# Kernel tuning notes

Hardware: AMD Instinct MI355X
Metric: run time of the kernel (lower is better)

## Reference

```python
import jax, jax.numpy as jnp
import numpy as np

N_NODES = 100000
N_EDGES = 1600000
IN_C, HID_C, OUT_C = 128, 256, 47


def setup_inputs() -> dict:
    key = jax.random.key(0)
    ks = jax.random.split(key, 8)
    x = jax.random.normal(ks[0], (N_NODES, IN_C), dtype=jnp.float32)
    edge_index = jax.random.randint(ks[1], (2, N_EDGES), 0, N_NODES, dtype=jnp.int64)

    def glorot(k, fan_in, fan_out):
        s = 1.0 / np.sqrt(fan_in)
        return jax.random.uniform(k, (fan_in, fan_out), jnp.float32, -s, s)

    W1_l = glorot(ks[2], IN_C, HID_C)
    b1 = jnp.zeros((HID_C,), jnp.float32)
    W1_r = glorot(ks[3], IN_C, HID_C)
    W2_l = glorot(ks[4], HID_C, OUT_C)
    b2 = jnp.zeros((OUT_C,), jnp.float32)
    W2_r = glorot(ks[5], HID_C, OUT_C)
    return {"x": x, "edge_index": edge_index,
            "W1_l": W1_l, "b1": b1, "W1_r": W1_r,
            "W2_l": W2_l, "b2": b2, "W2_r": W2_r}


def _sage_conv(x, src, dst, W_l, b, W_r, num_nodes):
    # mean aggregation of source-node features onto destination nodes
    msg_sum = jax.ops.segment_sum(x[src], dst, num_segments=num_nodes)  # [N, C]
    cnt = jax.ops.segment_sum(jnp.ones((src.shape[0], 1), x.dtype), dst,
                              num_segments=num_nodes)                   # [N, 1]
    mean = msg_sum / jnp.maximum(cnt, 1.0)
    # out = lin_l(mean) + lin_r(x_root); lin_l carries the bias (PyG default)
    return mean @ W_l + b + x @ W_r


def reference(x, edge_index, W1_l, b1, W1_r, W2_l, b2, W2_r):
    num_nodes = x.shape[0]
    src, dst = edge_index[0], edge_index[1]
    h = _sage_conv(x, src, dst, W1_l, b1, W1_r, num_nodes)
    h = jax.nn.relu(h)  # dropout is identity in eval mode
    out = _sage_conv(h, src, dst, W2_l, b2, W2_r, num_nodes)
    return jax.nn.log_softmax(out, axis=-1)
```

## Files before the change

kernel.cpp:

```cpp
#include <hip/hip_runtime.h>
#include <hip/hip_bf16.h>

constexpr int IN_C  = 128;
constexpr int HID_C = 256;
constexpr int OUT_C = 47;

typedef __attribute__((ext_vector_type(8))) short bf16x8;
typedef __attribute__((ext_vector_type(4))) float f32x4;

static __device__ __forceinline__ unsigned short f2bf(float v) {
  __hip_bfloat16 hb = __float2bfloat16(v);
  return *(unsigned short*)&hb;
}
static __device__ __forceinline__ float bf2f(unsigned short u) {
  return __uint_as_float((unsigned)u << 16);
}


__global__ __launch_bounds__(256) void count_edges(const int* __restrict__ dst,
                                                   int* __restrict__ cnt, int E) {
  int e = blockIdx.x * blockDim.x + threadIdx.x;
  const int stride = gridDim.x * blockDim.x;
  for (; e < E; e += stride) {
    const int d = __builtin_nontemporal_load(&dst[e]);
    atomicAdd(&cnt[d], 1);
  }
}

__global__ __launch_bounds__(256) void scan_partials(const int* __restrict__ cnt,
                                                     int* __restrict__ part, int N) {
  const int i0 = blockIdx.x * 1024 + threadIdx.x * 4;
  int s = 0;
  if (i0 + 3 < N) {
    const int4 v = *(const int4*)&cnt[i0];
    s = v.x + v.y + v.z + v.w;
  } else {
    for (int k = 0; k < 4; ++k) { const int i = i0 + k; if (i < N) s += cnt[i]; }
  }
  #pragma unroll
  for (int o = 32; o > 0; o >>= 1) s += __shfl_xor(s, o, 64);
  __shared__ int ws[4];
  if ((threadIdx.x & 63) == 0) ws[threadIdx.x >> 6] = s;
  __syncthreads();
  if (threadIdx.x == 0) part[blockIdx.x] = ws[0] + ws[1] + ws[2] + ws[3];
}

__global__ __launch_bounds__(1024) void scan_roots(int* __restrict__ part,
                                                   int* __restrict__ off, int nb, int N) {
  __shared__ int tmp[1024];
  const int t = threadIdx.x;
  const int v = (t < nb) ? part[t] : 0;
  tmp[t] = v;
  __syncthreads();
  for (int d = 1; d < 1024; d <<= 1) {
    const int u = (t >= d) ? tmp[t - d] : 0;
    __syncthreads();
    tmp[t] += u;
    __syncthreads();
  }
  if (t < nb) part[t] = tmp[t] - v;
  if (t == 1023) off[N] = tmp[1023];
}

__global__ __launch_bounds__(256) void scan_write(const int* __restrict__ cnt,
                                                  const int* __restrict__ part,
                                                  int* __restrict__ off, int N) {
  const int b = blockIdx.x;
  const int i0 = b * 1024 + threadIdx.x * 4;
  int4 v = make_int4(0, 0, 0, 0);
  if (i0 + 3 < N) v = *(const int4*)&cnt[i0];
  else {
    int* p = (int*)&v;
    for (int k = 0; k < 4; ++k) { const int i = i0 + k; if (i < N) p[k] = cnt[i]; }
  }
  const int tsum = v.x + v.y + v.z + v.w;
  const int lane = threadIdx.x & 63;
  int incl = tsum;
  #pragma unroll
  for (int o = 1; o < 64; o <<= 1) {
    const int u = __shfl_up(incl, o, 64);
    if (lane >= o) incl += u;
  }
  __shared__ int wsum[4];
  const int wv = threadIdx.x >> 6;
  if (lane == 63) wsum[wv] = incl;
  __syncthreads();
  int wbase = 0;
  for (int w = 0; w < wv; ++w) wbase += wsum[w];
  const int tbase = part[b] + wbase + incl - tsum;
  int4 ov;
  ov.x = tbase;
  ov.y = tbase + v.x;
  ov.z = tbase + v.x + v.y;
  ov.w = tbase + v.x + v.y + v.z;
  if (i0 + 3 < N) *(int4*)&off[i0] = ov;
  else {
    int* p = (int*)&ov;
    for (int k = 0; k < 4; ++k) { const int i = i0 + k; if (i < N) off[i] = p[k]; }
  }
}

__global__ __launch_bounds__(256) void fill_csr_range(const int* __restrict__ src,
                                                      const int* __restrict__ dst,
                                                      const int* __restrict__ off,
                                                      int* __restrict__ cursor,
                                                      int* __restrict__ csr,
                                                      int E, int lo, int hi) {
  int e = blockIdx.x * blockDim.x + threadIdx.x;
  const int stride = gridDim.x * blockDim.x;
  for (; e < E; e += stride) {
    const int d = __builtin_nontemporal_load(&dst[e]);
    if (d >= lo && d < hi) {
      const int s = __builtin_nontemporal_load(&src[e]);
      const int p = atomicAdd(&cursor[d], 1);
      csr[off[d] + p] = s;
    }
  }
}

__global__ void f32_to_bf16(const float* __restrict__ in, unsigned short* __restrict__ out, int n4) {
  int i = blockIdx.x * blockDim.x + threadIdx.x;
  if (i < n4) {
    float4 v = *(const float4*)&in[i * 4];
    ushort4 o;
    o.x = f2bf(v.x); o.y = f2bf(v.y); o.z = f2bf(v.z); o.w = f2bf(v.w);
    *(ushort4*)&out[i * 4] = o;
  }
}

__global__ __launch_bounds__(256) void agg1(const unsigned short* __restrict__ xb,
                                            const int* __restrict__ off,
                                            const int* __restrict__ csr,
                                            unsigned short* __restrict__ meanb, int N) {
  const int wid  = (blockIdx.x * blockDim.x + threadIdx.x) >> 6;
  const int lane = threadIdx.x & 63;
  if (wid >= N) return;
  const unsigned* xw = (const unsigned*)xb;
  const int s0 = off[wid], s1 = off[wid + 1];
  float a0 = 0.f, a1 = 0.f, b0 = 0.f, b1 = 0.f;
  float c0 = 0.f, c1 = 0.f, d0 = 0.f, d1 = 0.f;
  for (int base = s0; base < s1; base += 64) {
    const int cnt = min(64, s1 - base);
    const int idx = (lane < cnt) ? csr[base + lane] : 0;
    int e = 0;
    for (; e + 4 <= cnt; e += 4) {
      const int sA = __shfl(idx, e, 64),     sB = __shfl(idx, e + 1, 64);
      const int sC = __shfl(idx, e + 2, 64), sD = __shfl(idx, e + 3, 64);
      const unsigned uA = xw[(size_t)sA * 64 + lane];
      const unsigned uB = xw[(size_t)sB * 64 + lane];
      const unsigned uC = xw[(size_t)sC * 64 + lane];
      const unsigned uD = xw[(size_t)sD * 64 + lane];
      a0 += __uint_as_float(uA << 16); a1 += __uint_as_float(uA & 0xffff0000u);
      b0 += __uint_as_float(uB << 16); b1 += __uint_as_float(uB & 0xffff0000u);
      c0 += __uint_as_float(uC << 16); c1 += __uint_as_float(uC & 0xffff0000u);
      d0 += __uint_as_float(uD << 16); d1 += __uint_as_float(uD & 0xffff0000u);
    }
    for (; e < cnt; ++e) {
      const int sA = __shfl(idx, e, 64);
      const unsigned uA = xw[(size_t)sA * 64 + lane];
      a0 += __uint_as_float(uA << 16); a1 += __uint_as_float(uA & 0xffff0000u);
    }
  }
  const float r0 = (a0 + b0) + (c0 + d0);
  const float r1 = (a1 + b1) + (c1 + d1);
  const int deg = s1 - s0;
  const float inv = (deg > 0) ? 1.0f / (float)deg : 0.0f;
  const unsigned lo = f2bf(r0 * inv), hi = f2bf(r1 * inv);
  ((unsigned*)meanb)[(size_t)wid * 64 + lane] = lo | (hi << 16);
}

__global__ void build_w1cat_t(const float* __restrict__ Wl, const float* __restrict__ Wr,
                              unsigned short* __restrict__ BT) {
  int idx = blockIdx.x * blockDim.x + threadIdx.x;
  if (idx < 256 * 256) {
    int j = idx >> 8, k = idx & 255;
    float v = (k < 128) ? Wl[k * 256 + j] : Wr[(k - 128) * 256 + j];
    BT[idx] = f2bf(v);
  }
}
__global__ void build_w2cat_t(const float* __restrict__ Wl, const float* __restrict__ Wr,
                              unsigned short* __restrict__ BT) {
  int idx = blockIdx.x * blockDim.x + threadIdx.x;
  if (idx < 128 * 256) {
    int j = idx >> 8, k = idx & 255;
    float v = 0.f;
    if (j < OUT_C)           v = Wl[k * OUT_C + j];
    else if (j < 2 * OUT_C)  v = Wr[k * OUT_C + (j - OUT_C)];
    BT[idx] = f2bf(v);
  }
}

template<int MODE>
__global__ __launch_bounds__(256) void gemm_mfma(const unsigned short* __restrict__ A0,
                                                 const unsigned short* __restrict__ A1,
                                                 const unsigned short* __restrict__ BT,
                                                 const float* __restrict__ bias,
                                                 unsigned short* __restrict__ Out,
                                                 int M) {
  constexpr int ONC = (MODE == 0) ? 256 : 128;
  __shared__ unsigned short Asl[128 * 64];
  __shared__ unsigned short Bsl[128 * 64];
  const int tid  = threadIdx.x;
  const int wid  = tid >> 6, lane = tid & 63;
  const int wm   = wid >> 1, wn = wid & 1;
  const int r0   = blockIdx.x * 128;
  const int c0   = blockIdx.y * 128;

  f32x4 acc[4][4];
  #pragma unroll
  for (int m = 0; m < 4; ++m)
    #pragma unroll
    for (int n = 0; n < 4; ++n)
      #pragma unroll
      for (int j = 0; j < 4; ++j) acc[m][n][j] = 0.f;

  const int srow = lane >> 3;
  const int cs   = (lane & 7) ^ srow;
  const int fr   = lane & 15;
  const int klo  = (lane >> 4) * 16;
  const int swz  = (fr & 7) << 4;

  #pragma unroll 1
  for (int kb = 0; kb < 4; ++kb) {
    const unsigned short* Ap;
    int acol, ak;
    if (MODE == 0) { Ap = (kb < 2) ? A0 : A1; acol = (kb & 1) * 64; ak = 128; }
    else           { Ap = A0;                 acol = kb * 64;       ak = 256; }
    #pragma unroll
    for (int i = 0; i < 4; ++i) {
      const int rl = wid * 32 + i * 8 + srow;
      int gr = r0 + rl; if (gr > M - 1) gr = M - 1;
      const unsigned short* gsa = Ap + (size_t)gr * ak + acol + cs * 8;
      __builtin_amdgcn_global_load_lds(
          (const __attribute__((address_space(1))) unsigned int*)gsa,
          (__attribute__((address_space(3))) unsigned int*)&Asl[(wid * 32 + i * 8) * 64],
          16, 0, 0);
      const unsigned short* gsb = BT + (size_t)(c0 + rl) * 256 + kb * 64 + cs * 8;
      __builtin_amdgcn_global_load_lds(
          (const __attribute__((address_space(1))) unsigned int*)gsb,
          (__attribute__((address_space(3))) unsigned int*)&Bsl[(wid * 32 + i * 8) * 64],
          16, 0, 0);
    }
    asm volatile("s_waitcnt vmcnt(0)");
    __syncthreads();
    #pragma unroll
    for (int ks = 0; ks < 2; ++ks) {
      bf16x8 af[4], bfv[4];
      #pragma unroll
      for (int m = 0; m < 4; ++m) {
        const int ro = (wm * 64 + m * 16 + fr) * 128 + ((ks * 64 + klo) ^ swz);
        af[m] = *(const bf16x8*)((const char*)Asl + ro);
      }
      #pragma unroll
      for (int n = 0; n < 4; ++n) {
        const int ro = (wn * 64 + n * 16 + fr) * 128 + ((ks * 64 + klo) ^ swz);
        bfv[n] = *(const bf16x8*)((const char*)Bsl + ro);
      }
      #pragma unroll
      for (int m = 0; m < 4; ++m)
        #pragma unroll
        for (int n = 0; n < 4; ++n)
          acc[m][n] = __builtin_amdgcn_mfma_f32_16x16x32_bf16(af[m], bfv[n], acc[m][n], 0, 0, 0);
    }
    __syncthreads();
  }

  const int orow0 = r0 + wm * 64 + (lane >> 4) * 4;
  const int ocol0 = c0 + wn * 64 + (lane & 15);
  #pragma unroll
  for (int m = 0; m < 4; ++m) {
    #pragma unroll
    for (int n = 0; n < 4; ++n) {
      const int col = ocol0 + n * 16;
      const float badd = (MODE == 0) ? bias[col] : 0.f;
      #pragma unroll
      for (int j = 0; j < 4; ++j) {
        const int row = orow0 + m * 16 + j;
        if (row < M) {
          float v = acc[m][n][j] + badd;
          if (MODE == 0) v = fmaxf(v, 0.f);
          Out[(size_t)row * ONC + col] = f2bf(v);
        }
      }
    }
  }
}

__global__ __launch_bounds__(256) void final_kernel(const unsigned short* __restrict__ Ob,
                                                    const int* __restrict__ off,
                                                    const int* __restrict__ csr,
                                                    const float* __restrict__ b2,
                                                    float* __restrict__ out, int N) {
  const int wid  = (blockIdx.x * blockDim.x + threadIdx.x) >> 6;
  const int lane = threadIdx.x & 63;
  if (wid >= N) return;
  const int s0 = off[wid], s1 = off[wid + 1];
  const bool act = lane < OUT_C;
  const int cl = act ? lane : 0;
  float t0 = 0.f, t1 = 0.f, t2 = 0.f, t3 = 0.f;
  for (int base = s0; base < s1; base += 64) {
    const int cnt = min(64, s1 - base);
    const int idx = (lane < cnt) ? csr[base + lane] : 0;
    int e = 0;
    for (; e + 4 <= cnt; e += 4) {
      const int sA = __shfl(idx, e, 64),     sB = __shfl(idx, e + 1, 64);
      const int sC = __shfl(idx, e + 2, 64), sD = __shfl(idx, e + 3, 64);
      if (act) {
        t0 += bf2f(Ob[(size_t)sA * 128 + lane]);
        t1 += bf2f(Ob[(size_t)sB * 128 + lane]);
        t2 += bf2f(Ob[(size_t)sC * 128 + lane]);
        t3 += bf2f(Ob[(size_t)sD * 128 + lane]);
      }
    }
    for (; e < cnt; ++e) {
      const int sA = __shfl(idx, e, 64);
      if (act) t0 += bf2f(Ob[(size_t)sA * 128 + lane]);
    }
  }
  const float sum = (t0 + t1) + (t2 + t3);
  const int deg = s1 - s0;
  const float inv = (deg > 0) ? 1.0f / (float)deg : 0.0f;
  float v = sum * inv + b2[cl] + bf2f(Ob[(size_t)wid * 128 + OUT_C + cl]);
  if (!act) v = -INFINITY;
  float m = v;
  #pragma unroll
  for (int o = 32; o > 0; o >>= 1) m = fmaxf(m, __shfl_xor(m, o, 64));
  float ex = act ? expf(v - m) : 0.f;
  float s = ex;
  #pragma unroll
  for (int o = 32; o > 0; o >>= 1) s += __shfl_xor(s, o, 64);
  if (act) out[(size_t)wid * OUT_C + lane] = v - m - logf(s);
}


extern "C" void kernel_launch(void* const* d_in, const int* in_sizes, int n_in,
                              void* d_out, int out_size, void* d_ws, size_t ws_size,
                              hipStream_t stream) {
  const float* x   = (const float*)d_in[0];
  const int*   ei  = (const int*)d_in[1];
  const float* W1l = (const float*)d_in[2];
  const float* b1  = (const float*)d_in[3];
  const float* W1r = (const float*)d_in[4];
  const float* W2l = (const float*)d_in[5];
  const float* b2  = (const float*)d_in[6];
  const float* W2r = (const float*)d_in[7];
  float* out = (float*)d_out;

  const int N = in_sizes[0] / IN_C;
  const int E = in_sizes[1] / 2;
  const int* src = ei;
  const int* dst = ei + E;

  char* base = (char*)d_ws;
  size_t o = 0;
  auto take = [&](size_t bytes) -> char* {
    char* p = base + o;
    o = (o + bytes + 255) & ~(size_t)255;
    return p;
  };
  int* cnt    = (int*)take((size_t)N * 4);
  int* cursor = (int*)take((size_t)N * 4);
  const size_t zero_bytes = o;
  int* off    = (int*)take((size_t)(N + 1) * 4);
  int* part   = (int*)take((size_t)1024 * 4);
  int* csr    = (int*)take((size_t)E * 4);
  unsigned short* xb    = (unsigned short*)take((size_t)N * IN_C * 2);
  unsigned short* meanb = (unsigned short*)take((size_t)N * IN_C * 2);
  unsigned short* h     = (unsigned short*)take((size_t)N * HID_C * 2);
  unsigned short* W1T   = (unsigned short*)take((size_t)256 * 256 * 2);
  unsigned short* W2T   = (unsigned short*)take((size_t)128 * 256 * 2);
  unsigned short* Ocat  = meanb;
  (void)ws_size; (void)n_in; (void)out_size;

  hipMemsetAsync(base, 0, zero_bytes, stream);

  const int tb = 256;
  const int nb = (N + 1023) / 1024;
  count_edges<<<2048, tb, 0, stream>>>(dst, cnt, E);
  scan_partials<<<nb, 256, 0, stream>>>(cnt, part, N);
  scan_roots<<<1, 1024, 0, stream>>>(part, off, nb, N);
  scan_write<<<nb, 256, 0, stream>>>(cnt, part, off, N);

  const int P = 4;
  const int chunk = (N + P - 1) / P;
  for (int p = 0; p < P; ++p) {
    const int lo = p * chunk;
    const int hi = min(N, lo + chunk);
    fill_csr_range<<<2048, tb, 0, stream>>>(src, dst, off, cursor, csr, E, lo, hi);
  }

  const int n4 = N * IN_C / 4;
  f32_to_bf16<<<(n4 + tb - 1) / tb, tb, 0, stream>>>(x, xb, n4);
  build_w1cat_t<<<256, 256, 0, stream>>>(W1l, W1r, W1T);
  build_w2cat_t<<<128, 256, 0, stream>>>(W2l, W2r, W2T);

  agg1<<<(N + 3) / 4, 256, 0, stream>>>(xb, off, csr, meanb, N);

  const int mb = (N + 127) / 128;
  gemm_mfma<0><<<dim3(mb, 2), 256, 0, stream>>>(meanb, xb, W1T, b1, h, N);
  gemm_mfma<1><<<dim3(mb, 1), 256, 0, stream>>>(h, nullptr, W2T, nullptr, Ocat, N);

  final_kernel<<<(N + 3) / 4, 256, 0, stream>>>(Ocat, off, csr, b2, out, N);
}
```

Baseline: 475.9 us.

## Build CSR with LDS-privatized per-range histograms and block-local scatter cursors

Replaces the global-atomic edge count and the four-pass global-atomic CSR fill with a two-level scheme. Node ranges of 16384 are handled in shared memory, with 32 edge slices per range, so each block builds a private LDS histogram. A column-sum kernel turns these into per-block base offsets. The scatter kernel then uses LDS atomics on cursors seeded from the global offsets, which removes the memset and the global atomic contention. The cost is that every block rescans its whole edge slice for each of the 7 ranges, and a partial buffer of R*32*16384 ints is written and read back.

```diff
diff --git a/kernel.cpp b/kernel.cpp
--- a/kernel.cpp
+++ b/kernel.cpp
@@ -5,6 +5,9 @@
 constexpr int HID_C = 256;
 constexpr int OUT_C = 47;
 
+constexpr int RN  = 16384;
+constexpr int NB  = 32;
+
 typedef __attribute__((ext_vector_type(8))) short bf16x8;
 typedef __attribute__((ext_vector_type(4))) float f32x4;
 
@@ -16,14 +19,64 @@
   return __uint_as_float((unsigned)u << 16);
 }
 
-
-__global__ __launch_bounds__(256) void count_edges(const int* __restrict__ dst,
-                                                   int* __restrict__ cnt, int E) {
-  int e = blockIdx.x * blockDim.x + threadIdx.x;
-  const int stride = gridDim.x * blockDim.x;
-  for (; e < E; e += stride) {
+__global__ __launch_bounds__(256) void hist_kernel(const int* __restrict__ dst,
+                                                   int* __restrict__ partial,
+                                                   int N, int E) {
+  __shared__ int h[RN];
+  const int r = blockIdx.x / NB, b = blockIdx.x % NB;
+  const int lo = r * RN;
+  const int hi = min(N, lo + RN);
+  for (int i = threadIdx.x; i < RN; i += 256) h[i] = 0;
+  __syncthreads();
+  const int e0 = (int)((long long)E * b / NB);
+  const int e1 = (int)((long long)E * (b + 1) / NB);
+  for (int e = e0 + threadIdx.x; e < e1; e += 256) {
     const int d = __builtin_nontemporal_load(&dst[e]);
-    atomicAdd(&cnt[d], 1);
+    if (d >= lo && d < hi) atomicAdd(&h[d - lo], 1);
+  }
+  __syncthreads();
+  int* out = partial + (size_t)(r * NB + b) * RN;
+  for (int i = threadIdx.x; i < RN; i += 256) out[i] = h[i];
+}
+
+__global__ __launch_bounds__(256) void colsum_kernel(int* __restrict__ partial,
+                                                     int* __restrict__ cnt, int N) {
+  const int g = blockIdx.x * 256 + threadIdx.x;
+  if (g >= N) return;
+  const int r = g / RN, i = g % RN;
+  size_t idx = (size_t)(r * NB) * RN + i;
+  int run = 0;
+  for (int b = 0; b < NB; ++b, idx += RN) {
+    const int t = partial[idx];
+    partial[idx] = run;
+    run += t;
+  }
+  cnt[g] = run;
+}
+
+__global__ __launch_bounds__(256) void scatter_kernel(const int* __restrict__ src,
+                                                      const int* __restrict__ dst,
+                                                      const int* __restrict__ off,
+                                                      const int* __restrict__ partial,
+                                                      int* __restrict__ csr,
+                                                      int N, int E) {
+  __shared__ int cur[RN];
+  const int r = blockIdx.x / NB, b = blockIdx.x % NB;
+  const int lo = r * RN;
+  const int hi = min(N, lo + RN);
+  const int* pb = partial + (size_t)(r * NB + b) * RN;
+  for (int i = threadIdx.x; i < hi - lo; i += 256)
+    cur[i] = off[lo + i] + pb[i];
+  __syncthreads();
+  const int e0 = (int)((long long)E * b / NB);
+  const int e1 = (int)((long long)E * (b + 1) / NB);
+  for (int e = e0 + threadIdx.x; e < e1; e += 256) {
+    const int d = __builtin_nontemporal_load(&dst[e]);
+    if (d >= lo && d < hi) {
+      const int s = __builtin_nontemporal_load(&src[e]);
+      const int p = atomicAdd(&cur[d - lo], 1);
+      csr[p] = s;
+    }
   }
 }
 
@@ -97,24 +150,6 @@
   else {
     int* p = (int*)&ov;
     for (int k = 0; k < 4; ++k) { const int i = i0 + k; if (i < N) off[i] = p[k]; }
-  }
-}
-
-__global__ __launch_bounds__(256) void fill_csr_range(const int* __restrict__ src,
-                                                      const int* __restrict__ dst,
-                                                      const int* __restrict__ off,
-                                                      int* __restrict__ cursor,
-                                                      int* __restrict__ csr,
-                                                      int E, int lo, int hi) {
-  int e = blockIdx.x * blockDim.x + threadIdx.x;
-  const int stride = gridDim.x * blockDim.x;
-  for (; e < E; e += stride) {
-    const int d = __builtin_nontemporal_load(&dst[e]);
-    if (d >= lo && d < hi) {
-      const int s = __builtin_nontemporal_load(&src[e]);
-      const int p = atomicAdd(&cursor[d], 1);
-      csr[off[d] + p] = s;
-    }
   }
 }
 
@@ -350,6 +385,7 @@
   const int E = in_sizes[1] / 2;
   const int* src = ei;
   const int* dst = ei + E;
+  const int R = (N + RN - 1) / RN;
 
   char* base = (char*)d_ws;
   size_t o = 0;
@@ -359,11 +395,10 @@
     return p;
   };
   int* cnt    = (int*)take((size_t)N * 4);
-  int* cursor = (int*)take((size_t)N * 4);
-  const size_t zero_bytes = o;
   int* off    = (int*)take((size_t)(N + 1) * 4);
-  int* part   = (int*)take((size_t)1024 * 4);
+  int* spart  = (int*)take((size_t)1024 * 4);
   int* csr    = (int*)take((size_t)E * 4);
+  int* partial= (int*)take((size_t)R * NB * RN * 4);
   unsigned short* xb    = (unsigned short*)take((size_t)N * IN_C * 2);
   unsigned short* meanb = (unsigned short*)take((size_t)N * IN_C * 2);
   unsigned short* h     = (unsigned short*)take((size_t)N * HID_C * 2);
@@ -372,22 +407,15 @@
   unsigned short* Ocat  = meanb;
   (void)ws_size; (void)n_in; (void)out_size;
 
-  hipMemsetAsync(base, 0, zero_bytes, stream);
-
   const int tb = 256;
   const int nb = (N + 1023) / 1024;
-  count_edges<<<2048, tb, 0, stream>>>(dst, cnt, E);
-  scan_partials<<<nb, 256, 0, stream>>>(cnt, part, N);
-  scan_roots<<<1, 1024, 0, stream>>>(part, off, nb, N);
-  scan_write<<<nb, 256, 0, stream>>>(cnt, part, off, N);
-
-  const int P = 4;
-  const int chunk = (N + P - 1) / P;
-  for (int p = 0; p < P; ++p) {
-    const int lo = p * chunk;
-    const int hi = min(N, lo + chunk);
-    fill_csr_range<<<2048, tb, 0, stream>>>(src, dst, off, cursor, csr, E, lo, hi);
-  }
+
+  hist_kernel<<<R * NB, 256, 0, stream>>>(dst, partial, N, E);
+  colsum_kernel<<<(N + 255) / 256, 256, 0, stream>>>(partial, cnt, N);
+  scan_partials<<<nb, 256, 0, stream>>>(cnt, spart, N);
+  scan_roots<<<1, 1024, 0, stream>>>(spart, off, nb, N);
+  scan_write<<<nb, 256, 0, stream>>>(cnt, spart, off, N);
+  scatter_kernel<<<R * NB, 256, 0, stream>>>(src, dst, off, partial, csr, N, E);
 
   const int n4 = N * IN_C / 4;
   f32_to_bf16<<<(n4 + tb - 1) / tb, tb, 0, stream>>>(x, xb, n4);
```

After: 577.7 us. +21.4%, slower.
